# Optimization experiments

Hardware: AMD Instinct MI355X
Metric: run time of the kernel (lower is better)

The kernel has to match this reference:

```python
import jax, jax.numpy as jnp
import numpy as np

TEMPERATURE = 1.0
CHUNK = 128  # node-block size for the curvature pass


def setup_inputs() -> dict:
    key = jax.random.key(0)
    k1, k2 = jax.random.split(key)
    N, D = 4096, 64
    x = jax.random.normal(k1, (N, D), dtype=jnp.float32)
    # sparse binary adjacency (avg degree ~16) + ring so min degree >= 2
    A = (jax.random.uniform(k2, (N, N)) < 0.004).astype(jnp.float32)
    i = jnp.arange(N)
    A = A.at[i, i].set(0.0)
    A = A.at[i, (i + 1) % N].set(1.0)
    A = A.at[(i + 1) % N, i].set(1.0)
    return {"node_embeddings": x, "adj_matrix": A}


def _physics_components(x, A):
    N, d = x.shape
    mask = A > 0
    deg = jnp.sum(A, axis=-1)                      # [N]

    # ---- total energy ----
    kinetic = jnp.sum(x * x, axis=-1)
    nb = A @ x                                     # neighbor aggregate [N,d]
    potential = -jnp.sum(x * nb, axis=-1)
    total_energy = kinetic + potential / (deg + 1e-8)

    # ---- local entropy over neighbor similarities ----
    xn = x / jnp.maximum(jnp.linalg.norm(x, axis=-1, keepdims=True), 1e-12)
    S = xn @ xn.T                                  # cosine sims [N,N]
    logits = jnp.where(mask, S / TEMPERATURE, -1e30)
    P = jax.nn.softmax(logits, axis=-1)            # masked softmax per row
    local_entropy = -jnp.sum(jnp.where(mask, P * jnp.log(P + 1e-8), 0.0), axis=-1)

    # ---- equilibrium deviation (5-NN local mean in embedding space) ----
    sq = jnp.sum(x * x, axis=-1)
    D2 = jnp.maximum(sq[:, None] + sq[None, :] - 2.0 * (x @ x.T), 1e-12)
    dist = jnp.sqrt(D2)                            # [N,N]
    _, idx = jax.lax.top_k(-dist, 6)               # smallest 6 (self first)
    local_means = jnp.mean(x[idx[:, 1:]], axis=1)  # [N,d]
    gdev = jnp.linalg.norm(x - jnp.mean(x, axis=0, keepdims=True), axis=-1)
    ldev = jnp.linalg.norm(x - local_means, axis=-1)
    equilibrium_deviation = 0.6 * gdev + 0.4 * ldev

    # ---- structural centrality ----
    en = jnp.linalg.norm(x, axis=-1)
    structural_centrality = 0.5 * deg / (N - 1) + 0.5 * en / jnp.max(en)

    # ---- information flow: unbiased var of neighbor sims ----
    ms = jnp.sum(jnp.where(mask, S, 0.0), axis=-1) / deg
    information_flow = jnp.sum(jnp.where(mask, (S - ms[:, None]) ** 2, 0.0), axis=-1) / (deg - 1.0)

    # ---- stability: 1/(1 + mean unbiased var of neighbor embeddings) ----
    m1 = nb / deg[:, None]
    ex2 = A @ (x * x)
    var_dim = (ex2 - deg[:, None] * m1 * m1) / (deg - 1.0)[:, None]
    stability = 1.0 / (1.0 + jnp.mean(var_dim, axis=-1))

    # ---- discrete curvature: 1 - mean pairwise cos angle of centered neighbors ----
    # mean_{j<k} u_j.u_k = (||sum u||^2 - sum ||u||^2) / (deg*(deg-1))
    def body(_, ids):
        xb = x[ids]                                 # [B,d]
        mb = mask[ids]                              # [B,N]
        c = x[None, :, :] - xb[:, None, :]          # [B,N,d]
        nrm = jnp.sqrt(jnp.maximum(jnp.sum(c * c, -1), 1e-12))
        u = jnp.where(mb[..., None], c / jnp.maximum(nrm, 1e-8)[..., None], 0.0)
        s = jnp.sum(u, axis=1)                      # [B,d]
        ssq = jnp.sum(u * u, axis=(1, 2))           # [B]
        db = jnp.sum(mb.astype(x.dtype), axis=-1)
        mean_cos = (jnp.sum(s * s, -1) - ssq) / (db * (db - 1.0))
        return None, 1.0 - mean_cos

    _, curv = jax.lax.scan(body, None, jnp.arange(N).reshape(-1, CHUNK))
    graph_curvature = curv.reshape(N)

    return (total_energy, local_entropy, equilibrium_deviation,
            structural_centrality, information_flow, stability, graph_curvature)


def reference(node_embeddings, adj_matrix):
    return _physics_components(node_embeddings, adj_matrix)
```

## Files before the change

kernel.cpp:

```cpp
#include <hip/hip_runtime.h>
#include <math.h>

#define NN 4096
#define DD 64
#define NSPLIT 16
#define JW 256

typedef _Float16 half8 __attribute__((ext_vector_type(8)));
typedef float f32x4 __attribute__((ext_vector_type(4)));

__device__ __forceinline__ unsigned sxu(unsigned v, int o){
  return (unsigned)__shfl_xor((int)v, o, 64);
}
__device__ __forceinline__ unsigned umn(unsigned a, unsigned b){ return a<b?a:b; }
__device__ __forceinline__ unsigned umx(unsigned a, unsigned b){ return a<b?b:a; }

__device__ __forceinline__ unsigned packkey32(float m, int j){
  float q = fmaf(m, 2048.f, 524288.f);
  q = fminf(fmaxf(q, 0.f), 1048575.f);
  return (((unsigned)q) << 12) | (unsigned)j;
}

__device__ __forceinline__ void ins5u(unsigned k, unsigned b[5]){
  bool c0=k<b[0], c1=k<b[1], c2=k<b[2], c3=k<b[3], c4=k<b[4];
  b[4] = c3 ? b[3] : (c4 ? k : b[4]);
  b[3] = c2 ? b[2] : (c3 ? k : b[3]);
  b[2] = c1 ? b[1] : (c2 ? k : b[2]);
  b[1] = c0 ? b[0] : (c1 ? k : b[1]);
  b[0] = c0 ? k : b[0];
}

__device__ __forceinline__ void mergeStage32(unsigned b[5], int st){
  unsigned p0=sxu(b[0],st),p1=sxu(b[1],st),p2=sxu(b[2],st),p3=sxu(b[3],st),p4=sxu(b[4],st);
  unsigned o0=umn(b[0],p0);
  unsigned o1=umn(umn(b[1],p1), umx(b[0],p0));
  unsigned o2=umn(umn(b[2],p2), umn(umx(b[0],p1),umx(b[1],p0)));
  unsigned o3=umn(umn(b[3],p3), umn(umx(b[0],p2), umn(umx(b[1],p1),umx(b[2],p0))));
  unsigned o4=umn(umn(b[4],p4), umn(umn(umx(b[0],p3),umx(b[1],p2)),
                                    umn(umx(b[2],p1),umx(b[3],p0))));
  b[0]=o0;b[1]=o1;b[2]=o2;b[3]=o3;b[4]=o4;
}

__device__ __forceinline__ void mergeLocal32(const unsigned a[5], const unsigned c[5], unsigned b[5]){
  b[0]=umn(a[0],c[0]);
  b[1]=umn(umn(a[1],c[1]), umx(a[0],c[0]));
  b[2]=umn(umn(a[2],c[2]), umn(umx(a[0],c[1]),umx(a[1],c[0])));
  b[3]=umn(umn(a[3],c[3]), umn(umx(a[0],c[2]), umn(umx(a[1],c[1]),umx(a[2],c[0]))));
  b[4]=umn(umn(a[4],c[4]), umn(umn(umx(a[0],c[3]),umx(a[1],c[2])),
                               umn(umx(a[2],c[1]),umx(a[3],c[0]))));
}

__global__ __launch_bounds__(256) void k_prec(const float* __restrict__ x,
                      float* __restrict__ sq,
                      _Float16* __restrict__ xh, _Float16* __restrict__ xl,
                      float* __restrict__ msum_part, float* __restrict__ maxsq_part){
  __shared__ float part[4][64];
  __shared__ float mxp[4];
  const int w = threadIdx.x>>6, lane = threadIdx.x&63;
  const int n0 = blockIdx.x*16 + w*4;
  float v0 = x[(size_t)(n0+0)*DD + lane];
  float v1 = x[(size_t)(n0+1)*DD + lane];
  float v2 = x[(size_t)(n0+2)*DD + lane];
  float v3 = x[(size_t)(n0+3)*DD + lane];
  float s0=v0*v0, s1=v1*v1, s2=v2*v2, s3=v3*v3;
#pragma unroll
  for(int o=1;o<64;o<<=1){
    s0 += __shfl_xor(s0,o,64); s1 += __shfl_xor(s1,o,64);
    s2 += __shfl_xor(s2,o,64); s3 += __shfl_xor(s3,o,64);
  }
  float vv[4] = {v0,v1,v2,v3};
  float ss[4] = {s0,s1,s2,s3};
#pragma unroll
  for(int q=0;q<4;q++){
    float v = vv[q];
    _Float16 h = (_Float16)v;
    _Float16 l = (_Float16)(v - (float)h);
    xh[(size_t)(n0+q)*DD+lane] = h;
    xl[(size_t)(n0+q)*DD+lane] = l;
    if(lane==0) sq[n0+q]=ss[q];
  }
  if(lane==0) mxp[w] = fmaxf(fmaxf(s0,s1), fmaxf(s2,s3));
  part[w][lane] = v0+v1+v2+v3; __syncthreads();
  if(w==0){
    msum_part[blockIdx.x*64 + lane] = part[0][lane]+part[1][lane]+part[2][lane]+part[3][lane];
    if(lane==0) maxsq_part[blockIdx.x] = fmaxf(fmaxf(mxp[0],mxp[1]), fmaxf(mxp[2],mxp[3]));
  }
}

__device__ __forceinline__ f32x4 gram6(const half8 J[4],
    half8 Ih0, half8 Ih1, half8 Il0, half8 Il1){
  const f32x4 z = {0.f,0.f,0.f,0.f};
  f32x4 a1 = __builtin_amdgcn_mfma_f32_16x16x32_f16(J[0], Ih0, z, 0,0,0);
  f32x4 a2 = __builtin_amdgcn_mfma_f32_16x16x32_f16(J[2], Ih0, z, 0,0,0);
  a1 = __builtin_amdgcn_mfma_f32_16x16x32_f16(J[1], Ih1, a1, 0,0,0);
  a2 = __builtin_amdgcn_mfma_f32_16x16x32_f16(J[3], Ih1, a2, 0,0,0);
  a1 = __builtin_amdgcn_mfma_f32_16x16x32_f16(J[0], Il0, a1, 0,0,0);
  a1 = __builtin_amdgcn_mfma_f32_16x16x32_f16(J[1], Il1, a1, 0,0,0);
  return a1 + a2;
}

__global__ __launch_bounds__(256, 4) void k_mega(
    const float* __restrict__ x, const float* __restrict__ A,
    const float* __restrict__ sq,
    const _Float16* __restrict__ xh, const _Float16* __restrict__ xl,
    unsigned* __restrict__ cand,
    const float* __restrict__ msum_part, const float* __restrict__ maxsq_part,
    float* __restrict__ msum, float* __restrict__ max_sq, float* __restrict__ deg_out,
    float* __restrict__ o_te, float* __restrict__ o_ent,
    float* __restrict__ o_if, float* __restrict__ o_st, float* __restrict__ o_cv)
{
  __shared__ int   nbr[4][128];
  __shared__ float Sval[4][128];
  __shared__ float rr[4][64];
  __shared__ float rm[4];
  __shared__ _Float16 jHi[512*8];
  __shared__ _Float16 jLo[512*8];
  const int bid = blockIdx.x;
  const int tid = threadIdx.x;
  const int w = tid>>6, lane = tid&63;

  if(bid == 0){
    float s = 0.f;
    for(int p=w; p<256; p+=4) s += msum_part[p*64 + lane];
    rr[w][lane] = s;
    float m = maxsq_part[w*64 + lane];
#pragma unroll
    for(int o=1;o<64;o<<=1) m = fmaxf(m, __shfl_xor(m,o,64));
    if(lane==0) rm[w] = m;
    __syncthreads();
    if(w==0){
      msum[lane] = rr[0][lane]+rr[1][lane]+rr[2][lane]+rr[3][lane];
      if(lane==0) max_sq[0] = fmaxf(fmaxf(rm[0],rm[1]), fmaxf(rm[2],rm[3]));
    }
    return;
  }

  const int t = bid - 1;
  if((t & 1) == 0){
    const int i = (t>>1)*4 + w;
    const float xid = x[(size_t)i*DD + lane];
    const float sqi = sq[i];
    const float eni = sqrtf(sqi);
    const float4* A4 = (const float4*)(A + (size_t)i*NN);
    const unsigned long long below = (1ull << lane) - 1ull;

    int base = 0;
#define COMPACT(VAL, JJ) { \
    bool p_ = (VAL) > 0.f; \
    unsigned long long m_ = __ballot(p_); \
    int ofs_ = base + (int)__popcll(m_ & below); \
    if(p_ && ofs_ < 128) nbr[w][ofs_] = (JJ); \
    base += (int)__popcll(m_); \
  }
    for(int ch=0; ch<4; ++ch){
      float4 av[4];
#pragma unroll
      for(int qq=0; qq<4; ++qq) av[qq] = A4[lane + 64*(ch*4+qq)];
#pragma unroll
      for(int qq=0; qq<4; ++qq){
        int jb = 4*(lane + 64*(ch*4+qq));
        COMPACT(av[qq].x, jb+0);
        COMPACT(av[qq].y, jb+1);
        COMPACT(av[qq].z, jb+2);
        COMPACT(av[qq].w, jb+3);
      }
    }
#undef COMPACT
    const int deg = base;

    const float degf = (float)deg;
    const int dmax = min(deg, 128);
    float nb_d=0.f, ex2_d=0.f, s_d=0.f, ssq=0.f;

    for(int c0=0; c0<dmax; c0+=8){
      int jq[8]; float aq[8], qq[8];
#pragma unroll
      for(int q=0;q<8;q++) jq[q] = nbr[w][min(c0+q, dmax-1)];
#pragma unroll
      for(int q=0;q<8;q++) aq[q] = x[(size_t)jq[q]*DD + lane];
#pragma unroll
      for(int q=0;q<8;q++) qq[q] = sq[jq[q]];
      asm volatile("" :: "v"(aq[0]), "v"(aq[1]), "v"(aq[2]), "v"(aq[3]),
                         "v"(aq[4]), "v"(aq[5]), "v"(aq[6]), "v"(aq[7]));
      float p[8];
#pragma unroll
      for(int q=0;q<8;q++) p[q] = xid*aq[q];
#pragma unroll
      for(int o=1;o<64;o<<=1){
#pragma unroll
        for(int q=0;q<8;q++) p[q] += __shfl_xor(p[q],o,64);
      }
#pragma unroll
      for(int q=0;q<8;q++){
        const bool valid = (c0+q) < deg;
        float c2 = fmaxf(sqi + qq[q] - 2.0f*p[q], 1e-12f);
        float inv = 1.0f/fmaxf(sqrtf(c2), 1e-8f);
        nb_d  += valid ? aq[q] : 0.f;
        ex2_d += valid ? aq[q]*aq[q] : 0.f;
        s_d   += valid ? (aq[q]-xid)*inv : 0.f;
        ssq   += valid ? c2*inv*inv : 0.f;
        if(valid && lane==q) Sval[w][c0+q] = p[q]/(eni*sqrtf(qq[q]));
      }
    }

    float t0 = xid*nb_d;
    float m1 = nb_d/degf;
    float t1 = (ex2_d - degf*m1*m1)/(degf-1.0f);
    float t2 = s_d*s_d;
    float t3 = 0.f, t4 = 0.f;
    for(int s=lane; s<dmax; s+=64){ float v=Sval[w][s]; t3 += expf(v); t4 += v; }
#pragma unroll
    for(int o=1;o<64;o<<=1){
      t0 += __shfl_xor(t0,o,64); t1 += __shfl_xor(t1,o,64); t2 += __shfl_xor(t2,o,64);
      t3 += __shfl_xor(t3,o,64); t4 += __shfl_xor(t4,o,64);
    }
    const float pot = t0, varm = t1*(1.0f/DD), s2 = t2, se = t3, ms = t4/degf;

    float e0=0.f, e1=0.f;
    const float inv_se = 1.0f/se;
    for(int s=lane; s<dmax; s+=64){
      float v = Sval[w][s];
      float pp = expf(v)*inv_se;
      e0 -= pp*logf(pp + 1e-8f);
      float dv = v-ms; e1 += dv*dv;
    }
#pragma unroll
    for(int o=1;o<64;o<<=1){ e0 += __shfl_xor(e0,o,64); e1 += __shfl_xor(e1,o,64); }

    if(lane==0){
      o_te[i]  = sqi - pot/(degf + 1e-8f);
      o_ent[i] = e0;
      o_if[i]  = e1/(degf-1.0f);
      o_st[i]  = 1.0f/(1.0f + varm);
      o_cv[i]  = 1.0f - (s2 - ssq)/(degf*(degf-1.0f));
      deg_out[i] = degf;
    }
  } else {
    const int kid = t >> 1;
    const int split = kid & (NSPLIT-1);
    const int strip = (kid >> 4)*4 + w;
    const int ibase = strip*16, j0 = split*JW;
    const int col = lane & 15, kg = lane >> 4;
    const int vo = col*DD + kg*8;
    const int myi = ibase + col;

#define STAGE(CH) { \
    _Pragma("unroll") \
    for(int q_=0;q_<2;q_++){ \
      int g_ = q_*256 + tid; \
      int r_ = g_ >> 3; \
      int c_ = (g_ & 7) ^ (r_ & 7); \
      const _Float16* sH_ = xh + (size_t)(j0 + (CH)*64 + r_)*DD + c_*8; \
      const _Float16* sL_ = xl + (size_t)(j0 + (CH)*64 + r_)*DD + c_*8; \
      __builtin_amdgcn_global_load_lds( \
        (const __attribute__((address_space(1))) unsigned int*)sH_, \
        (__attribute__((address_space(3))) unsigned int*)(jHi + g_*8), 16, 0, 0); \
      __builtin_amdgcn_global_load_lds( \
        (const __attribute__((address_space(1))) unsigned int*)sL_, \
        (__attribute__((address_space(3))) unsigned int*)(jLo + g_*8), 16, 0, 0); \
    } }

    const _Float16* pih = xh + (size_t)ibase*DD + vo;
    const _Float16* pil = xl + (size_t)ibase*DD + vo;
    const half8 Ih0 = *(const half8*)(pih);
    const half8 Ih1 = *(const half8*)(pih+32);
    const half8 Il0 = *(const half8*)(pil);
    const half8 Il1 = *(const half8*)(pil+32);

    unsigned bA[5], bB[5];
#pragma unroll
    for(int k=0;k<5;k++){ bA[k]=0xFFFFFFFFu; bB[k]=0xFFFFFFFFu; }

#pragma unroll
    for(int ch=0; ch<4; ch++){
      STAGE(ch);
      const int jb0 = j0 + ch*64 + kg*4;
      float4 sq0 = *(const float4*)(sq + jb0);
      float4 sq1 = *(const float4*)(sq + jb0 + 16);
      float4 sq2 = *(const float4*)(sq + jb0 + 32);
      float4 sq3 = *(const float4*)(sq + jb0 + 48);
      __syncthreads();

      half8 JT[4];
#define TILE(TT, SQV, LIST) { \
      const int rl_ = (TT)*16 + col; \
      const int sw_ = rl_ & 7; \
      JT[0] = *(const half8*)(jHi + (rl_*8 + ( kg      ^ sw_))*8); \
      JT[1] = *(const half8*)(jHi + (rl_*8 + ((kg + 4) ^ sw_))*8); \
      JT[2] = *(const half8*)(jLo + (rl_*8 + ( kg      ^ sw_))*8); \
      JT[3] = *(const half8*)(jLo + (rl_*8 + ((kg + 4) ^ sw_))*8); \
      f32x4 d_ = gram6(JT, Ih0, Ih1, Il0, Il1); \
      float sv_[4] = {SQV.x, SQV.y, SQV.z, SQV.w}; \
      const int jt0_ = jb0 + (TT)*16; \
      _Pragma("unroll") \
      for(int r_=0;r_<4;r_++){ \
        unsigned kk_ = packkey32(fmaf(-2.0f, d_[r_], sv_[r_]), jt0_+r_); \
        kk_ = (jt0_+r_==myi) ? 0xFFFFFFFFu : kk_; \
        ins5u(kk_, LIST); \
      } }

      TILE(0, sq0, bA);
      TILE(1, sq1, bB);
      TILE(2, sq2, bA);
      TILE(3, sq3, bB);
#undef TILE
      __syncthreads();
    }
#undef STAGE

    unsigned b[5];
    mergeLocal32(bA, bB, b);
    mergeStage32(b, 16);
    mergeStage32(b, 32);

    if(kg==0){
#pragma unroll
      for(int k=0;k<5;k++)
        cand[((size_t)myi*NSPLIT + split)*5 + k] = b[k];
    }
  }
}

__global__ __launch_bounds__(256) void k_nnsel(
    const float* __restrict__ x, const unsigned* __restrict__ cand,
    const float* __restrict__ msum, const float* __restrict__ max_sq,
    const float* __restrict__ deg, const float* __restrict__ sq,
    float* __restrict__ o_eq, float* __restrict__ o_sc)
{
  const int w = threadIdx.x>>6, l = threadIdx.x&63;
  const int i = blockIdx.x*4 + w;
  const unsigned* cr = cand + (size_t)i*(NSPLIT*5);
  unsigned c0 = cr[l];
  unsigned c1 = (l < 16) ? cr[64+l] : 0xFFFFFFFFu;

  int sel[5];
#pragma unroll
  for(int k=0;k<5;k++){
    unsigned d = umn(c0,c1);
#pragma unroll
    for(int o=1;o<64;o<<=1) d = umn(d, sxu(d,o));
    sel[k] = (int)(d & 0xFFFu);
    if(c0==d) c0=0xFFFFFFFFu;
    else if(c1==d) c1=0xFFFFFFFFu;
  }

  float smv=0.f;
#pragma unroll
  for(int k=0;k<5;k++) smv += x[(size_t)sel[k]*DD + l];
  float xiv = x[(size_t)i*DD + l];
  float lv = xiv - smv*0.2f;
  float gv = xiv - msum[l]*(1.0f/NN);
  float pl = lv*lv, pg = gv*gv;
#pragma unroll
  for(int o=1;o<64;o<<=1){ pl += __shfl_xor(pl,o,64); pg += __shfl_xor(pg,o,64); }
  if(l==0){
    o_eq[i] = 0.6f*sqrtf(pg) + 0.4f*sqrtf(pl);
    o_sc[i] = 0.5f*deg[i]/(float)(NN-1) + 0.5f*sqrtf(sq[i])/sqrtf(max_sq[0]);
  }
}

extern "C" void kernel_launch(void* const* d_in, const int* in_sizes, int n_in,
                              void* d_out, int out_size, void* d_ws, size_t ws_size,
                              hipStream_t stream) {
  const float* x = (const float*)d_in[0];
  const float* A = (const float*)d_in[1];
  float* out = (float*)d_out;
  float* ws  = (float*)d_ws;
  float*     sq        = ws;
  float*     msum      = ws + 4096;
  float*     max_sq    = ws + 4160;
  float*     deg       = ws + 4224;
  float*     msum_part = ws + 8320;
  float*     maxsq_part= ws + 24704;
  _Float16*  xh        = (_Float16*)(ws + 24960);
  _Float16*  xl        = (_Float16*)(ws + 156032);
  unsigned*  cand      = (unsigned*)(ws + 287104);

  k_prec<<<NN/16, 256, 0, stream>>>(x, sq, xh, xl, msum_part, maxsq_part);
  k_mega<<<NN/2 + 1, 256, 0, stream>>>(x, A, sq, xh, xl, cand,
                                       msum_part, maxsq_part, msum, max_sq, deg,
                                       out, out+NN, out+4*NN, out+5*NN, out+6*NN);
  k_nnsel<<<NN/4, 256, 0, stream>>>(x, cand, msum, max_sq, deg, sq,
                                    out+2*NN, out+3*NN);
}
```

Before: 56.79 us.

## Use med3/min3 instructions for top-5 insertion and alias shared memory across branches

Rewrites the sorted top-5 insertion as v_med3_u32 operations, and the merge networks as v_min3_u32, cutting the instruction count in the kNN selection path. It also replaces the separate per-branch shared arrays with one 16KB union buffer that each block role carves up. Less LDS per block may allow more resident blocks per CU. Inline asm can restrict compiler scheduling.

Result: no change. 57.45 us (+1.2%).

```diff
diff --git a/kernel.cpp b/kernel.cpp
--- a/kernel.cpp
+++ b/kernel.cpp
@@ -14,6 +14,12 @@
 }
 __device__ __forceinline__ unsigned umn(unsigned a, unsigned b){ return a<b?a:b; }
 __device__ __forceinline__ unsigned umx(unsigned a, unsigned b){ return a<b?b:a; }
+__device__ __forceinline__ unsigned med3u(unsigned a, unsigned b, unsigned c){
+  unsigned r; asm("v_med3_u32 %0, %1, %2, %3" : "=v"(r) : "v"(a), "v"(b), "v"(c)); return r;
+}
+__device__ __forceinline__ unsigned min3u(unsigned a, unsigned b, unsigned c){
+  unsigned r; asm("v_min3_u32 %0, %1, %2, %3" : "=v"(r) : "v"(a), "v"(b), "v"(c)); return r;
+}
 
 __device__ __forceinline__ unsigned packkey32(float m, int j){
   float q = fmaf(m, 2048.f, 524288.f);
@@ -22,32 +28,32 @@
 }
 
 __device__ __forceinline__ void ins5u(unsigned k, unsigned b[5]){
-  bool c0=k<b[0], c1=k<b[1], c2=k<b[2], c3=k<b[3], c4=k<b[4];
-  b[4] = c3 ? b[3] : (c4 ? k : b[4]);
-  b[3] = c2 ? b[2] : (c3 ? k : b[3]);
-  b[2] = c1 ? b[1] : (c2 ? k : b[2]);
-  b[1] = c0 ? b[0] : (c1 ? k : b[1]);
-  b[0] = c0 ? k : b[0];
+  unsigned nb0 = umn(k, b[0]);
+  b[4] = med3u(k, b[3], b[4]);
+  b[3] = med3u(k, b[2], b[3]);
+  b[2] = med3u(k, b[1], b[2]);
+  b[1] = med3u(k, b[0], b[1]);
+  b[0] = nb0;
 }
 
 __device__ __forceinline__ void mergeStage32(unsigned b[5], int st){
   unsigned p0=sxu(b[0],st),p1=sxu(b[1],st),p2=sxu(b[2],st),p3=sxu(b[3],st),p4=sxu(b[4],st);
   unsigned o0=umn(b[0],p0);
-  unsigned o1=umn(umn(b[1],p1), umx(b[0],p0));
-  unsigned o2=umn(umn(b[2],p2), umn(umx(b[0],p1),umx(b[1],p0)));
-  unsigned o3=umn(umn(b[3],p3), umn(umx(b[0],p2), umn(umx(b[1],p1),umx(b[2],p0))));
-  unsigned o4=umn(umn(b[4],p4), umn(umn(umx(b[0],p3),umx(b[1],p2)),
-                                    umn(umx(b[2],p1),umx(b[3],p0))));
+  unsigned o1=min3u(b[1],p1, umx(b[0],p0));
+  unsigned o2=min3u(b[2],p2, umn(umx(b[0],p1),umx(b[1],p0)));
+  unsigned o3=min3u(b[3],p3, min3u(umx(b[0],p2), umx(b[1],p1), umx(b[2],p0)));
+  unsigned o4=min3u(b[4],p4, umn(umn(umx(b[0],p3),umx(b[1],p2)),
+                                 umn(umx(b[2],p1),umx(b[3],p0))));
   b[0]=o0;b[1]=o1;b[2]=o2;b[3]=o3;b[4]=o4;
 }
 
 __device__ __forceinline__ void mergeLocal32(const unsigned a[5], const unsigned c[5], unsigned b[5]){
   b[0]=umn(a[0],c[0]);
-  b[1]=umn(umn(a[1],c[1]), umx(a[0],c[0]));
-  b[2]=umn(umn(a[2],c[2]), umn(umx(a[0],c[1]),umx(a[1],c[0])));
-  b[3]=umn(umn(a[3],c[3]), umn(umx(a[0],c[2]), umn(umx(a[1],c[1]),umx(a[2],c[0]))));
-  b[4]=umn(umn(a[4],c[4]), umn(umn(umx(a[0],c[3]),umx(a[1],c[2])),
-                               umn(umx(a[2],c[1]),umx(a[3],c[0]))));
+  b[1]=min3u(a[1],c[1], umx(a[0],c[0]));
+  b[2]=min3u(a[2],c[2], umn(umx(a[0],c[1]),umx(a[1],c[0])));
+  b[3]=min3u(a[3],c[3], min3u(umx(a[0],c[2]), umx(a[1],c[1]), umx(a[2],c[0])));
+  b[4]=min3u(a[4],c[4], umn(umn(umx(a[0],c[3]),umx(a[1],c[2])),
+                            umn(umx(a[2],c[1]),umx(a[3],c[0]))));
 }
 
 __global__ __launch_bounds__(256) void k_prec(const float* __restrict__ x,
@@ -109,27 +115,24 @@
     float* __restrict__ o_te, float* __restrict__ o_ent,
     float* __restrict__ o_if, float* __restrict__ o_st, float* __restrict__ o_cv)
 {
-  __shared__ int   nbr[4][128];
-  __shared__ float Sval[4][128];
-  __shared__ float rr[4][64];
-  __shared__ float rm[4];
-  __shared__ _Float16 jHi[512*8];
-  __shared__ _Float16 jLo[512*8];
+  __shared__ __align__(16) char smem[16384];
   const int bid = blockIdx.x;
   const int tid = threadIdx.x;
   const int w = tid>>6, lane = tid&63;
 
   if(bid == 0){
+    float* rr = (float*)smem;
+    float* rm = (float*)(smem + 1024);
     float s = 0.f;
     for(int p=w; p<256; p+=4) s += msum_part[p*64 + lane];
-    rr[w][lane] = s;
+    rr[w*64 + lane] = s;
     float m = maxsq_part[w*64 + lane];
 #pragma unroll
     for(int o=1;o<64;o<<=1) m = fmaxf(m, __shfl_xor(m,o,64));
     if(lane==0) rm[w] = m;
     __syncthreads();
     if(w==0){
-      msum[lane] = rr[0][lane]+rr[1][lane]+rr[2][lane]+rr[3][lane];
+      msum[lane] = rr[0*64+lane]+rr[1*64+lane]+rr[2*64+lane]+rr[3*64+lane];
       if(lane==0) max_sq[0] = fmaxf(fmaxf(rm[0],rm[1]), fmaxf(rm[2],rm[3]));
     }
     return;
@@ -137,6 +140,8 @@
 
   const int t = bid - 1;
   if((t & 1) == 0){
+    int*   nbrw  = (int*)smem + w*128;
+    float* Svalw = (float*)(smem + 2048) + w*128;
     const int i = (t>>1)*4 + w;
     const float xid = x[(size_t)i*DD + lane];
     const float sqi = sq[i];
@@ -149,7 +154,7 @@
     bool p_ = (VAL) > 0.f; \
     unsigned long long m_ = __ballot(p_); \
     int ofs_ = base + (int)__popcll(m_ & below); \
-    if(p_ && ofs_ < 128) nbr[w][ofs_] = (JJ); \
+    if(p_ && ofs_ < 128) nbrw[ofs_] = (JJ); \
     base += (int)__popcll(m_); \
   }
     for(int ch=0; ch<4; ++ch){
@@ -175,7 +180,7 @@
     for(int c0=0; c0<dmax; c0+=8){
       int jq[8]; float aq[8], qq[8];
 #pragma unroll
-      for(int q=0;q<8;q++) jq[q] = nbr[w][min(c0+q, dmax-1)];
+      for(int q=0;q<8;q++) jq[q] = nbrw[min(c0+q, dmax-1)];
 #pragma unroll
       for(int q=0;q<8;q++) aq[q] = x[(size_t)jq[q]*DD + lane];
 #pragma unroll
@@ -199,7 +204,7 @@
         ex2_d += valid ? aq[q]*aq[q] : 0.f;
         s_d   += valid ? (aq[q]-xid)*inv : 0.f;
         ssq   += valid ? c2*inv*inv : 0.f;
-        if(valid && lane==q) Sval[w][c0+q] = p[q]/(eni*sqrtf(qq[q]));
+        if(valid && lane==q) Svalw[c0+q] = p[q]/(eni*sqrtf(qq[q]));
       }
     }
 
@@ -208,7 +213,7 @@
     float t1 = (ex2_d - degf*m1*m1)/(degf-1.0f);
     float t2 = s_d*s_d;
     float t3 = 0.f, t4 = 0.f;
-    for(int s=lane; s<dmax; s+=64){ float v=Sval[w][s]; t3 += expf(v); t4 += v; }
+    for(int s=lane; s<dmax; s+=64){ float v=Svalw[s]; t3 += expf(v); t4 += v; }
 #pragma unroll
     for(int o=1;o<64;o<<=1){
       t0 += __shfl_xor(t0,o,64); t1 += __shfl_xor(t1,o,64); t2 += __shfl_xor(t2,o,64);
@@ -219,7 +224,7 @@
     float e0=0.f, e1=0.f;
     const float inv_se = 1.0f/se;
     for(int s=lane; s<dmax; s+=64){
-      float v = Sval[w][s];
+      float v = Svalw[s];
       float pp = expf(v)*inv_se;
       e0 -= pp*logf(pp + 1e-8f);
       float dv = v-ms; e1 += dv*dv;
@@ -236,6 +241,8 @@
       deg_out[i] = degf;
     }
   } else {
+    _Float16* jHi = (_Float16*)smem;
+    _Float16* jLo = (_Float16*)(smem + 8192);
     const int kid = t >> 1;
     const int split = kid & (NSPLIT-1);
     const int strip = (kid >> 4)*4 + w;
```
